# Optimization experiments

Hardware: AMD Instinct MI355X
Metric: run time of the kernel (lower is better)

The kernel has to match this reference:

```python
import jax, jax.numpy as jnp
import numpy as np

B, E = 256, 512
C, K = 8192, 10          # n_class, n_center
LMD = 10.0
INV_GAMMA = 10.0         # 1 / gamma, gamma = 0.1
TAU = 0.2
MARGIN = 0.01


def setup_inputs() -> dict:
    key = jax.random.key(0)
    k1, k2, k3 = jax.random.split(key, 3)
    embeddings = jax.random.normal(k1, (B, E), dtype=jnp.float32)
    labels = jax.random.randint(k2, (B,), 0, C, dtype=jnp.int64)
    fc = jax.random.normal(k3, (C * K, E), dtype=jnp.float32)
    return {"embeddings": embeddings, "labels": labels, "fc": fc}


def reference(embeddings, labels, fc):
    # L2-normalize centers (rows of fc), like F.normalize(fc, p=2, dim=1)
    norm = jnp.sqrt(jnp.sum(fc * fc, axis=1, keepdims=True))
    w = fc / jnp.maximum(norm, 1e-12)

    # similarity to every center: [B, C, K]
    x = (embeddings @ w.T).reshape(B, C, K)
    prob = jax.nn.softmax(INV_GAMMA * x, axis=2)
    h = jnp.sum(prob * x, axis=2)  # [B, C] soft-pooled class similarity

    # subtract margin on ground-truth class, then cross-entropy
    rows = jnp.arange(B)
    margin_m = jnp.zeros_like(h).at[rows, labels].set(MARGIN)
    logits = LMD * (h - margin_m)
    logp = jax.nn.log_softmax(logits, axis=1)
    loss_cls = -jnp.mean(logp[rows, labels])

    # regularizer: batched per-class center gram, replaces python loop over C
    wc = w.reshape(C, K, E)
    sub = 1.0 - jnp.einsum('cke,cje->ckj', wc, wc)   # [C, K, K]
    sub = jnp.where(sub <= 0.0, 1e-10, sub)
    mask = jnp.triu(jnp.ones((K, K), dtype=bool), k=1)  # strict upper triangle
    safe = jnp.where(mask, 2.0 * sub, 1.0)
    reg = jnp.sum(jnp.where(mask, jnp.sqrt(safe), 0.0))
    reg = reg / (C * K * (K - 1.0))
    return loss_cls + TAU * reg
```

## Files before the change

### kernel.cpp

```cpp
#include <hip/hip_runtime.h>


typedef __bf16 bf16;
typedef bf16 bf16x8 __attribute__((ext_vector_type(8)));
typedef float f32x4 __attribute__((ext_vector_type(4)));

#define NCLASS 8192
#define KC 10
#define EDIM 512
#define BATCH 256

__device__ inline void load_lds16(const void* g, void* l) {
    __builtin_amdgcn_global_load_lds(
        (const __attribute__((address_space(1))) void*)g,
        (__attribute__((address_space(3))) void*)l, 16, 0, 0);
}

__global__ __launch_bounds__(256) void conv_kernel(
    const float* __restrict__ e, bf16* __restrict__ out)
{
    int i = blockIdx.x * 256 + threadIdx.x;
    float4 a = ((const float4*)e)[i * 2];
    float4 b = ((const float4*)e)[i * 2 + 1];
    bf16x8 v;
    v[0] = (bf16)a.x; v[1] = (bf16)a.y; v[2] = (bf16)a.z; v[3] = (bf16)a.w;
    v[4] = (bf16)b.x; v[5] = (bf16)b.y; v[6] = (bf16)b.z; v[7] = (bf16)b.w;
    ((bf16x8*)out)[i] = v;
}

__global__ __launch_bounds__(512, 2) void fused_kernel(
    const float* __restrict__ fc,
    const bf16* __restrict__ A,
    float* __restrict__ h,
    float* __restrict__ gram_part)
{
    __shared__ bf16 Wl[80 * EDIM];
    __shared__ bf16 Es[256 * 32];
    const int tid = threadIdx.x;
    const int wave = tid >> 6, lane = tid & 63;

    const int c = blockIdx.x * 8 + wave;
    float4 ra[KC][2];
    #pragma unroll
    for (int r = 0; r < KC; ++r) {
        const float4* rp =
            (const float4*)(fc + ((size_t)c * KC + r) * EDIM) + lane * 2;
        ra[r][0] = rp[0];
        ra[r][1] = rp[1];
    }
    float invn[KC];
    #pragma unroll
    for (int r = 0; r < KC; ++r) {
        float4 a = ra[r][0], b = ra[r][1];
        float s = a.x*a.x + a.y*a.y + a.z*a.z + a.w*a.w
                + b.x*b.x + b.y*b.y + b.z*b.z + b.w*b.w;
        #pragma unroll
        for (int off = 32; off; off >>= 1) s += __shfl_xor(s, off);
        invn[r] = 1.0f / fmaxf(sqrtf(s), 1e-12f);
    }
    float part = 0.f;
    #pragma unroll
    for (int i = 0; i < KC - 1; ++i) {
        #pragma unroll
        for (int j = i + 1; j < KC; ++j) {
            float4 ai = ra[i][0], bi = ra[i][1];
            float4 aj = ra[j][0], bj = ra[j][1];
            float s = ai.x*aj.x + ai.y*aj.y + ai.z*aj.z + ai.w*aj.w
                    + bi.x*bj.x + bi.y*bj.y + bi.z*bj.z + bi.w*bj.w;
            #pragma unroll
            for (int off = 32; off; off >>= 1) s += __shfl_xor(s, off);
            float sub = 1.0f - s * invn[i] * invn[j];
            if (sub <= 0.0f) sub = 1e-10f;
            part += sqrtf(2.0f * sub);
        }
    }
    if (lane == 0) gram_part[c] = part;

    #pragma unroll
    for (int r = 0; r < KC; ++r) {
        int row = wave * KC + r;
        float inv = invn[r];
        float4 a = ra[r][0], b = ra[r][1];
        bf16x8 v;
        v[0] = (bf16)(a.x * inv); v[1] = (bf16)(a.y * inv);
        v[2] = (bf16)(a.z * inv); v[3] = (bf16)(a.w * inv);
        v[4] = (bf16)(b.x * inv); v[5] = (bf16)(b.y * inv);
        v[6] = (bf16)(b.z * inv); v[7] = (bf16)(b.w * inv);
        *(bf16x8*)&Wl[row * EDIM + ((lane ^ (row & 7)) << 3)] = v;
    }

    f32x4 acc[5][2];
    #pragma unroll
    for (int mt = 0; mt < 5; ++mt)
        #pragma unroll
        for (int nt = 0; nt < 2; ++nt)
            acc[mt][nt] = (f32x4){0.f, 0.f, 0.f, 0.f};

    const int srow = lane >> 2;
    const int scol = (lane & 3) * 8;

    for (int kb = 0; kb < EDIM; kb += 32) {
        #pragma unroll
        for (int p = 0; p < 2; ++p) {
            int row = p * 128 + wave * 16 + srow;
            load_lds16(A + row * EDIM + kb + scol,
                       Es + (p * 128 + wave * 16) * 32);
        }
        __syncthreads();

        const int q8 = (lane >> 4) * 8;
        const int fr = lane & 15;
        bf16x8 wf[5], ef[2];
        #pragma unroll
        for (int mt = 0; mt < 5; ++mt) {
            int row = mt * 16 + fr;
            wf[mt] = *(const bf16x8*)
                &Wl[row * EDIM + ((kb + q8) ^ ((row & 7) << 3))];
        }
        #pragma unroll
        for (int nt = 0; nt < 2; ++nt)
            ef[nt] = *(const bf16x8*)&Es[(wave * 32 + nt * 16 + fr) * 32 + q8];
        #pragma unroll
        for (int mt = 0; mt < 5; ++mt)
            #pragma unroll
            for (int nt = 0; nt < 2; ++nt)
                acc[mt][nt] = __builtin_amdgcn_mfma_f32_16x16x32_bf16(
                    wf[mt], ef[nt], acc[mt][nt], 0, 0, 0);
        __syncthreads();
    }

    const int col = lane & 15;
    const int quad = lane >> 4;
    const int cb = blockIdx.x * 8;
    #pragma unroll
    for (int nt = 0; nt < 2; ++nt) {
        int b = wave * 32 + nt * 16 + col;
        float hval[8];
        #pragma unroll
        for (int cc = 0; cc < 8; ++cc) {
            float xm = -1e30f;
            #pragma unroll
            for (int mt = 0; mt < 5; ++mt) {
                if (10 * cc + 10 > 16 * mt && 10 * cc < 16 * mt + 16) {
                    #pragma unroll
                    for (int rg = 0; rg < 4; ++rg) {
                        int r = 16 * mt + 4 * quad + rg;
                        if (r >= 10 * cc && r < 10 * cc + 10)
                            xm = fmaxf(xm, acc[mt][nt][rg]);
                    }
                }
            }
            xm = fmaxf(xm, __shfl_xor(xm, 16));
            xm = fmaxf(xm, __shfl_xor(xm, 32));
            float s1 = 0.f, s2 = 0.f;
            #pragma unroll
            for (int mt = 0; mt < 5; ++mt) {
                if (10 * cc + 10 > 16 * mt && 10 * cc < 16 * mt + 16) {
                    #pragma unroll
                    for (int rg = 0; rg < 4; ++rg) {
                        int r = 16 * mt + 4 * quad + rg;
                        if (r >= 10 * cc && r < 10 * cc + 10) {
                            float x = acc[mt][nt][rg];
                            float e = __expf(10.0f * (x - xm));
                            s1 += e; s2 += e * x;
                        }
                    }
                }
            }
            s1 += __shfl_xor(s1, 16); s1 += __shfl_xor(s1, 32);
            s2 += __shfl_xor(s2, 16); s2 += __shfl_xor(s2, 32);
            hval[cc] = s2 / s1;
        }
        if (quad == 0) {
            float4 v0 = {hval[0], hval[1], hval[2], hval[3]};
            float4 v1 = {hval[4], hval[5], hval[6], hval[7]};
            float4* dst = (float4*)&h[(size_t)b * NCLASS + cb];
            dst[0] = v0;
            dst[1] = v1;
        }
    }
}

__global__ __launch_bounds__(256) void ce_kernel(
    const float* __restrict__ h, const int* __restrict__ labels,
    float* __restrict__ ce_part)
{
    __shared__ float redm[4];
    __shared__ float reds[4];
    const int b = blockIdx.x, t = threadIdx.x;
    const int wave = t >> 6, lane = t & 63;
    const int lbl = labels[b];
    const float* hb = h + (size_t)b * NCLASS;

    float lg_cache[32];
    float mx = -1e30f;
    #pragma unroll
    for (int k = 0; k < 32; ++k) {
        int c = t + k * 256;
        float lg = 10.0f * hb[c];
        if (c == lbl) lg -= 0.1f;
        lg_cache[k] = lg;
        mx = fmaxf(mx, lg);
    }
    #pragma unroll
    for (int off = 32; off; off >>= 1) mx = fmaxf(mx, __shfl_xor(mx, off));
    if (lane == 0) redm[wave] = mx;
    __syncthreads();
    mx = fmaxf(fmaxf(redm[0], redm[1]), fmaxf(redm[2], redm[3]));

    float s = 0.f;
    #pragma unroll
    for (int k = 0; k < 32; ++k) s += __expf(lg_cache[k] - mx);
    #pragma unroll
    for (int off = 32; off; off >>= 1) s += __shfl_xor(s, off);
    if (lane == 0) reds[wave] = s;
    __syncthreads();
    if (t == 0) {
        s = reds[0] + reds[1] + reds[2] + reds[3];
        float logit_l = 10.0f * (hb[lbl] - 0.01f);
        ce_part[b] = mx + logf(s) - logit_l;
    }
}

__global__ __launch_bounds__(256) void final_kernel(
    const float* __restrict__ gram_part, const float* __restrict__ ce_part,
    float* __restrict__ out)
{
    __shared__ float red[4];
    const int t = threadIdx.x, wave = t >> 6, lane = t & 63;
    float g = 0.f;
    #pragma unroll
    for (int i = 0; i < 32; ++i) g += gram_part[t + i * 256];
    float val = ce_part[t] * (1.0f / 256.0f)
              + g * (0.2f / 737280.0f);
    #pragma unroll
    for (int off = 32; off; off >>= 1) val += __shfl_xor(val, off);
    if (lane == 0) red[wave] = val;
    __syncthreads();
    if (t == 0) out[0] = red[0] + red[1] + red[2] + red[3];
}

extern "C" void kernel_launch(void* const* d_in, const int* in_sizes, int n_in,
                              void* d_out, int out_size, void* d_ws, size_t ws_size,
                              hipStream_t stream) {
    const float* emb    = (const float*)d_in[0];
    const int*   labels = (const int*)d_in[1];
    const float* fc     = (const float*)d_in[2];
    float* out = (float*)d_out;

    char* ws = (char*)d_ws;
    bf16*  embb      = (bf16*)ws;
    float* h         = (float*)(ws + 262144);
    float* gram_part = (float*)(ws + 8650752);
    float* ce_part   = (float*)(ws + 8683520);

    conv_kernel<<<64, 256, 0, stream>>>(emb, embb);
    fused_kernel<<<NCLASS / 8, 512, 0, stream>>>(fc, embb, h, gram_part);
    ce_kernel<<<BATCH, 256, 0, stream>>>(h, labels, ce_part);
    final_kernel<<<1, 256, 0, stream>>>(gram_part, ce_part, out);
}
```

Measured before the change: 323.0 us.

## Read embedding fragments directly from global in k-blocked layout, drop LDS staging

The conversion kernel now writes the bf16 embeddings in a k-block-major layout (32-wide K slices, rows contiguous), so each wave can load its MFMA B fragments straight from global/L2 with contiguous 16-byte loads. The per-iteration LDS staging buffer and both barriers in the K loop are removed, leaving one barrier after the W tile is written. Launch bounds are raised to 4 blocks per CU to allow more occupancy. In exchange, every wave re-reads the embedding from L2 with no LDS sharing, and the higher occupancy target may force register spills given the large fp32 register footprint.

After: 345.1 us. 6.8% more time.

```diff
diff --git a/kernel.cpp b/kernel.cpp
--- a/kernel.cpp
+++ b/kernel.cpp
@@ -10,32 +10,27 @@
 #define EDIM 512
 #define BATCH 256
 
-__device__ inline void load_lds16(const void* g, void* l) {
-    __builtin_amdgcn_global_load_lds(
-        (const __attribute__((address_space(1))) void*)g,
-        (__attribute__((address_space(3))) void*)l, 16, 0, 0);
-}
-
 __global__ __launch_bounds__(256) void conv_kernel(
-    const float* __restrict__ e, bf16* __restrict__ out)
+    const float* __restrict__ e, bf16* __restrict__ At)
 {
     int i = blockIdx.x * 256 + threadIdx.x;
+    int row = i >> 6, chunk = i & 63;
+    int k = chunk * 8;
     float4 a = ((const float4*)e)[i * 2];
     float4 b = ((const float4*)e)[i * 2 + 1];
     bf16x8 v;
     v[0] = (bf16)a.x; v[1] = (bf16)a.y; v[2] = (bf16)a.z; v[3] = (bf16)a.w;
     v[4] = (bf16)b.x; v[5] = (bf16)b.y; v[6] = (bf16)b.z; v[7] = (bf16)b.w;
-    ((bf16x8*)out)[i] = v;
-}
-
-__global__ __launch_bounds__(512, 2) void fused_kernel(
+    *(bf16x8*)&At[((k >> 5) << 13) + (row << 5) + (k & 31)] = v;
+}
+
+__global__ __launch_bounds__(512, 4) void fused_kernel(
     const float* __restrict__ fc,
-    const bf16* __restrict__ A,
+    const bf16* __restrict__ At,
     float* __restrict__ h,
     float* __restrict__ gram_part)
 {
     __shared__ bf16 Wl[80 * EDIM];
-    __shared__ bf16 Es[256 * 32];
     const int tid = threadIdx.x;
     const int wave = tid >> 6, lane = tid & 63;
 
@@ -88,6 +83,7 @@
         v[6] = (bf16)(b.z * inv); v[7] = (bf16)(b.w * inv);
         *(bf16x8*)&Wl[row * EDIM + ((lane ^ (row & 7)) << 3)] = v;
     }
+    __syncthreads();
 
     f32x4 acc[5][2];
     #pragma unroll
@@ -96,21 +92,17 @@
         for (int nt = 0; nt < 2; ++nt)
             acc[mt][nt] = (f32x4){0.f, 0.f, 0.f, 0.f};
 
-    const int srow = lane >> 2;
-    const int scol = (lane & 3) * 8;
+    const int q8 = (lane >> 4) * 8;
+    const int fr = lane & 15;
 
     for (int kb = 0; kb < EDIM; kb += 32) {
-        #pragma unroll
-        for (int p = 0; p < 2; ++p) {
-            int row = p * 128 + wave * 16 + srow;
-            load_lds16(A + row * EDIM + kb + scol,
-                       Es + (p * 128 + wave * 16) * 32);
-        }
-        __syncthreads();
-
-        const int q8 = (lane >> 4) * 8;
-        const int fr = lane & 15;
         bf16x8 wf[5], ef[2];
+        #pragma unroll
+        for (int nt = 0; nt < 2; ++nt) {
+            int row = wave * 32 + nt * 16 + fr;
+            ef[nt] = *(const bf16x8*)
+                &At[((kb >> 5) << 13) + (row << 5) + q8];
+        }
         #pragma unroll
         for (int mt = 0; mt < 5; ++mt) {
             int row = mt * 16 + fr;
@@ -118,15 +110,11 @@
                 &Wl[row * EDIM + ((kb + q8) ^ ((row & 7) << 3))];
         }
         #pragma unroll
-        for (int nt = 0; nt < 2; ++nt)
-            ef[nt] = *(const bf16x8*)&Es[(wave * 32 + nt * 16 + fr) * 32 + q8];
-        #pragma unroll
         for (int mt = 0; mt < 5; ++mt)
             #pragma unroll
             for (int nt = 0; nt < 2; ++nt)
                 acc[mt][nt] = __builtin_amdgcn_mfma_f32_16x16x32_bf16(
                     wf[mt], ef[nt], acc[mt][nt], 0, 0, 0);
-        __syncthreads();
     }
 
     const int col = lane & 15;
@@ -249,13 +237,13 @@
     float* out = (float*)d_out;
 
     char* ws = (char*)d_ws;
-    bf16*  embb      = (bf16*)ws;
+    bf16*  At        = (bf16*)ws;
     float* h         = (float*)(ws + 262144);
     float* gram_part = (float*)(ws + 8650752);
     float* ce_part   = (float*)(ws + 8683520);
 
-    conv_kernel<<<64, 256, 0, stream>>>(emb, embb);
-    fused_kernel<<<NCLASS / 8, 512, 0, stream>>>(fc, embb, h, gram_part);
+    conv_kernel<<<64, 256, 0, stream>>>(emb, At);
+    fused_kernel<<<NCLASS / 8, 512, 0, stream>>>(fc, At, h, gram_part);
     ce_kernel<<<BATCH, 256, 0, stream>>>(h, labels, ce_part);
     final_kernel<<<1, 256, 0, stream>>>(gram_part, ce_part, out);
 }
```
